# Optimization experiments

Measured on AMD Instinct MI355X. Metric: run time of the kernel, lower is better.

The kernel has to match this reference:

```python
import jax, jax.numpy as jnp
import numpy as np

NUM_FEATURE = 512
HIDDEN = 256
NUM_CLASSES = 10
L1 = 1e-4
ALPHA = 1e-3
BATCH = 65536


def setup_inputs() -> dict:
    key = jax.random.key(0)
    k = jax.random.split(key, 6)
    x = jax.random.normal(k[0], (BATCH, NUM_FEATURE), dtype=jnp.float32)
    y = jax.random.randint(k[1], (BATCH,), 0, NUM_CLASSES, dtype=jnp.int32)
    fc0 = jax.random.normal(k[2], (NUM_FEATURE, 512), dtype=jnp.float32) / NUM_FEATURE
    fc1 = jax.random.normal(k[3], (NUM_FEATURE, 512), dtype=jnp.float32) / NUM_FEATURE
    w = jax.random.normal(k[4], (NUM_FEATURE, HIDDEN), dtype=jnp.float32) / NUM_FEATURE
    w1 = jax.random.normal(k[5], (HIDDEN, NUM_CLASSES), dtype=jnp.float32) / HIDDEN
    return {"x": x, "y": y, "fc0": fc0, "fc1": fc1, "w": w, "w1": w1}


def reference(x, y, fc0, fc1, w, w1):
    # sigmoid-gated MLP block with residual
    x1 = x @ fc0                                   # [B, 512]
    x2 = jax.nn.relu(x @ fc1)                      # [B, 512]
    x4 = x + (1.0 + jax.nn.sigmoid(x1)) * x2       # [B, 512] residual

    # head (Dropout(p=0.0) is identity)
    logits = jax.nn.relu(x4 @ w) @ w1              # [B, 10]
    pred = jnp.argmax(logits, axis=1)

    # cross-entropy (mean over batch)
    logp = jax.nn.log_softmax(logits, axis=-1)
    ce = -jnp.mean(jnp.take_along_axis(logp, y[:, None].astype(jnp.int32), axis=1))

    # L1 penalty on all weight matrices
    l1_pen = L1 * (jnp.abs(w1).sum() + jnp.abs(w).sum()
                   + jnp.abs(fc0).sum() + jnp.abs(fc1).sum())

    # per-class variance: sum_i ||mean_{y_i} - x4_i||^2, vectorized via segment sums
    counts = jax.ops.segment_sum(jnp.ones((x4.shape[0],), jnp.float32), y,
                                 num_segments=NUM_CLASSES)
    sums = jax.ops.segment_sum(x4, y, num_segments=NUM_CLASSES)   # [10, 512]
    means = sums / jnp.maximum(counts, 1.0)[:, None]
    var_loss = jnp.sum(jnp.square(means[y] - x4))

    loss = ce + l1_pen + ALPHA * var_loss
    acc = jnp.mean((pred.astype(jnp.int32) == y.astype(jnp.int32)).astype(jnp.float32))
    return (loss, acc)
```

## Files before the change

### kernel.cpp

```cpp
#include <hip/hip_runtime.h>
#include <stdint.h>

#define BATCH 65536
#define FDIM 512
#define HDIM 256
#define NC 10
#define NREP 16

typedef short short8 __attribute__((ext_vector_type(8)));
typedef float f32x4 __attribute__((ext_vector_type(4)));

#define OFF_FC0T   ((size_t)0)
#define OFF_FC1T   (OFF_FC0T + (size_t)512*512*2)
#define OFF_WT     (OFF_FC1T + (size_t)512*512*2)
#define OFF_XT     (OFF_WT   + (size_t)256*512*2)
#define OFF_X4T    (OFF_XT   + (size_t)BATCH*512*2)
#define OFF_ACC    (OFF_X4T  + (size_t)BATCH*512*2)
#define SCAL_SUMSQ 0
#define SCAL_CE    16
#define SCAL_ACC   32
#define SCAL_L1    48
#define SCAL_N     128
#define CNT_OFF    SCAL_N
#define GSUM_OFF   (SCAL_N + NREP*16)
#define ACC_FLOATS (GSUM_OFF + NREP*5120)
#define OFF_W1T    (OFF_ACC + (size_t)ACC_FLOATS*4)

#define GLL(g,l) __builtin_amdgcn_global_load_lds((const __attribute__((address_space(1))) void*)(g), (__attribute__((address_space(3))) void*)(l), 16, 0, 0)

__device__ __forceinline__ unsigned short f2b(float f){
  unsigned u = __float_as_uint(f);
  u += 0x7FFFu + ((u >> 16) & 1u);
  return (unsigned short)(u >> 16);
}
__device__ __forceinline__ float b2f(unsigned short h){
  return __uint_as_float(((unsigned)h) << 16);
}
__device__ __forceinline__ unsigned pk2b(float f0, float f1){
  unsigned u0 = __float_as_uint(f0) + 0x8000u;
  unsigned u1 = __float_as_uint(f1) + 0x8000u;
  return __builtin_amdgcn_perm(u1, u0, 0x07060302u);
}

__global__ __launch_bounds__(256) void k_setup(
    const float* __restrict__ x,   const float* __restrict__ fc0,
    const float* __restrict__ fc1, const float* __restrict__ w,
    const float* __restrict__ w1,
    unsigned short* __restrict__ xT,   unsigned short* __restrict__ fc0T,
    unsigned short* __restrict__ fc1T, unsigned short* __restrict__ wT,
    unsigned short* __restrict__ w1T,  float* __restrict__ accb)
{
  int blk = blockIdx.x, t = threadIdx.x;
  if (blk < 1024){
    int I = blk*4 + (t >> 6);
    int l = t & 63;
    int row = I*16 + (l & 15), q = l >> 4;
    const float* src = x + (size_t)row*FDIM + q*8;
    #pragma unroll
    for (int C = 0; C < 16; ++C){
      float4 v0 = *(const float4*)(src + C*32);
      float4 v1 = *(const float4*)(src + C*32 + 4);
      unsigned o[4];
      o[0] = pk2b(v0.x, v0.y); o[1] = pk2b(v0.z, v0.w);
      o[2] = pk2b(v1.x, v1.y); o[3] = pk2b(v1.z, v1.w);
      *(short8*)&xT[(((size_t)I*16 + C) << 9) + l*8] = *(short8*)o;
    }
    return;
  }
  if (blk < 1360){
    int i = (blk - 1024)*256 + t;
    float l1v = 0.f;
    if (i < 32768){
      int n4 = i&15, m = (i>>4)&3, C = (i>>6)&15, J = i>>10;
      int n = J*16+n4, k8 = C*4+m;
      unsigned short o[8];
      #pragma unroll
      for (int j=0;j<8;++j){ float v = fc0[(size_t)(k8*8+j)*512 + n]; o[j]=f2b(v); l1v += fabsf(v); }
      *(short8*)&fc0T[(size_t)(J*16+C)*512 + (i&63)*8] = *(short8*)o;
    } else if (i < 65536){
      int j0 = i - 32768;
      int n4 = j0&15, m = (j0>>4)&3, C = (j0>>6)&15, J = j0>>10;
      int n = J*16+n4, k8 = C*4+m;
      unsigned short o[8];
      #pragma unroll
      for (int j=0;j<8;++j){ float v = fc1[(size_t)(k8*8+j)*512 + n]; o[j]=f2b(v); l1v += fabsf(v); }
      *(short8*)&fc1T[(size_t)(J*16+C)*512 + (j0&63)*8] = *(short8*)o;
    } else if (i < 81920){
      int j0 = i - 65536;
      int n4 = j0&15, m = (j0>>4)&3, C = (j0>>6)&15, J = j0>>10;
      int n = J*16+n4, k8 = C*4+m;
      unsigned short o[8];
      #pragma unroll
      for (int j=0;j<8;++j){ float v = w[(size_t)(k8*8+j)*256 + n]; o[j]=f2b(v); l1v += fabsf(v); }
      *(short8*)&wT[(size_t)(J*16+C)*512 + (j0&63)*8] = *(short8*)o;
    } else if (i < 86016){
      int j0 = i - 81920;
      int C = j0 >> 9, l = (j0 >> 3) & 63, e = j0 & 7;
      int n = l & 15, k = C*32 + (l>>4)*8 + e;
      float v = (n < NC) ? w1[k*NC + n] : 0.f;
      w1T[C*512 + l*8 + e] = f2b(v);
      if (n < NC) l1v = fabsf(v);
    }
    for (int off = 32; off; off >>= 1) l1v += __shfl_down(l1v, off);
    if ((t & 63) == 0 && l1v != 0.f)
      atomicAdd(&accb[SCAL_L1 + (blk & (NREP-1))], l1v);
    return;
  }
  {
    int base = (blk - 1360)*1024;
    #pragma unroll
    for (int j=0;j<4;++j){
      int idx = base + j*256 + t;
      if (idx < ACC_FLOATS) accb[idx] = 0.f;
    }
  }
}


#define BARRIER() __builtin_amdgcn_s_barrier()
#define LGKM0() do{ asm volatile("s_waitcnt lgkmcnt(0)" ::: "memory"); \
                    __builtin_amdgcn_sched_barrier(0); }while(0)

#define READA(A, AB, H) do{                                                   \
  _Pragma("unroll") for (int c_=0;c_<2;++c_)                                  \
  _Pragma("unroll") for (int m_=0;m_<4;++m_)                                  \
    A[c_][m_] = *(const short8*)((AB) + (((wr*8 + (H)*4 + m_)*2 + c_)<<10) + lane*16); \
}while(0)

#define READB(B, BB, MAT) do{                                                 \
  _Pragma("unroll") for (int c_=0;c_<2;++c_)                                  \
  _Pragma("unroll") for (int n_=0;n_<2;++n_)                                  \
    B[c_][n_] = *(const short8*)((BB) + (MAT)*16384 + (((wc*2+n_)*2 + c_)<<10) + lane*16); \
}while(0)

#define MM(ACC, MB, A, B) do{                                                 \
  __builtin_amdgcn_s_setprio(1);                                              \
  _Pragma("unroll") for (int c_=0;c_<2;++c_)                                  \
  _Pragma("unroll") for (int n_=0;n_<2;++n_)                                  \
  _Pragma("unroll") for (int m_=0;m_<4;++m_)                                  \
    ACC[(MB)+m_][n_] = __builtin_amdgcn_mfma_f32_16x16x32_bf16(A[c_][m_], B[c_][n_], ACC[(MB)+m_][n_], 0,0,0); \
  __builtin_amdgcn_s_setprio(0);                                              \
}while(0)

#define STAGEA(KT2, H) do{                                                    \
  char* d_ = ldsd + (((KT2)&1) ? 65536 : 0);                                  \
  _Pragma("unroll") for (int r_=0;r_<2;++r_){                                 \
    int idx_ = r_*8 + wv, q_ = idx_>>1, C_ = idx_&1;                          \
    int Il_ = (q_&3) + ((q_>>2)<<3) + (H)*4;                                  \
    GLL(xb + (((size_t)((rowblk*16 + Il_)*16 + (KT2)*2 + C_)) << 10) + lane*16, \
        d_ + ((Il_*2 + C_) << 10) + lane*16);                                 \
  } }while(0)

#define STAGEB(KT2, MAT) do{                                                  \
  char* d_ = ldsd + (((KT2)&1) ? 65536 : 0) + 32768 + (MAT)*16384;            \
  const char* s_ = (MAT) ? b1b : b0b;                                         \
  _Pragma("unroll") for (int r_=0;r_<2;++r_){                                 \
    int idx_ = r_*8 + wv, J_ = idx_>>1, C_ = idx_&1;                          \
    GLL(s_ + (((size_t)((colblk*8 + J_)*16 + (KT2)*2 + C_)) << 10) + lane*16, \
        d_ + ((J_*2 + C_) << 10) + lane*16);                                  \
  } }while(0)

__global__ __launch_bounds__(512, 2) void k_gemm12(
    const unsigned short* __restrict__ xT,
    const unsigned short* __restrict__ fc0T,
    const unsigned short* __restrict__ fc1T,
    unsigned short* __restrict__ x4T,
    float* __restrict__ scal)
{
  extern __shared__ __align__(16) char ldsd[];

  int blk = blockIdx.x;
  int wg = (blk & 7)*128 + (blk >> 3);
  int rowblk = wg >> 2;
  int colblk = wg & 3;

  int t = threadIdx.x;
  int wv = t >> 6, lane = t & 63, ln = lane & 15, quad = lane >> 4;
  int wr = wv >> 2, wc = wv & 3;

  const char* xb  = (const char*)xT;
  const char* b0b = (const char*)fc0T;
  const char* b1b = (const char*)fc1T;

  const f32x4 zv = {0.f,0.f,0.f,0.f};
  f32x4 acc1[8][2], acc2[8][2];
  #pragma unroll
  for (int m=0;m<8;++m){ acc1[m][0]=zv; acc1[m][1]=zv; acc2[m][0]=zv; acc2[m][1]=zv; }

  STAGEA(0,0); STAGEA(0,1); STAGEB(0,0); STAGEB(0,1);
  STAGEB(1,0); STAGEA(1,1);
  asm volatile("s_waitcnt vmcnt(4)" ::: "memory");
  __builtin_amdgcn_sched_barrier(0);
  BARRIER();

  short8 a0[2][4], a1[2][4], bb[2][2];

  for (int kt = 0; kt < 8; ++kt){
    char* Ab = ldsd + ((kt&1) ? 65536 : 0);
    char* Bb = Ab + 32768;

    READA(a0, Ab, 0);
    READB(bb, Bb, 0);
    if (kt < 7) STAGEA(kt+1, 0);
    BARRIER(); LGKM0();
    MM(acc1, 0, a0, bb);
    BARRIER();

    READA(a1, Ab, 1);
    if (kt < 7) STAGEB(kt+1, 1);
    BARRIER(); LGKM0();
    MM(acc1, 4, a1, bb);
    BARRIER();

    READB(bb, Bb, 1);
    if (kt < 6) STAGEB(kt+2, 0);
    BARRIER(); LGKM0();
    MM(acc2, 4, a1, bb);
    BARRIER();

    READA(a0, Ab, 0);
    if (kt < 6) STAGEA(kt+2, 1);
    BARRIER(); LGKM0();
    MM(acc2, 0, a0, bb);
    if (kt < 6)       { asm volatile("s_waitcnt vmcnt(4)" ::: "memory"); }
    else if (kt == 6) { asm volatile("s_waitcnt vmcnt(0)" ::: "memory"); }
    __builtin_amdgcn_sched_barrier(0);
    BARRIER();
  }

  {
    int Cres = colblk*4 + wc;
    #pragma unroll
    for (int i = 0; i < 8; ++i){
      GLL(xb + (((size_t)((rowblk*16 + wr*8 + i)*16 + Cres)) << 10) + lane*16,
          ldsd + ((wv*8 + i) << 10) + lane*16);
    }
    asm volatile("s_waitcnt vmcnt(0)" ::: "memory");
  }
  __syncthreads();

  unsigned short* resU = (unsigned short*)ldsd;
  unsigned short* x4U  = (unsigned short*)(ldsd + 65536);
  float sumsq = 0.f;
  #pragma unroll
  for (int m = 0; m < 8; ++m){
    #pragma unroll
    for (int n = 0; n < 2; ++n){
      #pragma unroll
      for (int r = 0; r < 4; ++r){
        int slot = (quad*4 + r) | ((n*2 + (ln>>3)) << 4);
        int idx = ((wv*8 + m) << 9) + slot*8 + (ln & 7);
        float xv  = b2f(resU[idx]);
        float x1v = acc1[m][n][r];
        float x2v = fmaxf(acc2[m][n][r], 0.f);
        float gate = 1.f + 1.f/(1.f + __expf(-x1v));
        float x4v = fmaf(gate, x2v, xv);
        unsigned short ub = f2b(x4v);
        float fq = b2f(ub);
        sumsq = fmaf(fq, fq, sumsq);
        x4U[idx] = ub;
      }
    }
  }
  for (int off = 32; off; off >>= 1) sumsq += __shfl_down(sumsq, off);
  __syncthreads();
  float* red = (float*)ldsd;
  if (lane == 0) red[wv] = sumsq;
  __syncthreads();
  if (t == 0){
    float s = 0.f;
    #pragma unroll
    for (int i=0;i<8;++i) s += red[i];
    atomicAdd(&scal[SCAL_SUMSQ + (blk & (NREP-1))], s);
  }
  #pragma unroll
  for (int r = 0; r < 2; ++r){
    int o = r*512 + t;
    int tile = o >> 6, off16 = o & 63;
    int wvp = tile >> 3, i = tile & 7;
    size_t Ig = (size_t)rowblk*16 + (wvp>>2)*8 + i;
    int Cg = colblk*4 + (wvp & 3);
    *(short8*)&x4T[((Ig*16 + Cg) << 9) + off16*8] =
      *(const short8*)&x4U[(tile << 9) + off16*8];
  }
}

__global__ __launch_bounds__(256) void k_csum(const unsigned short* __restrict__ x4T,
                                              const int* __restrict__ y,
                                              float* __restrict__ gsum){
  int w = blockIdx.x*4 + (threadIdx.x >> 6);
  int l = threadIdx.x & 63;
  int C = w & 15, Ig = w >> 4;
  int rl = l & 15, q = l >> 4;
  float a[NC][8];
  #pragma unroll
  for (int c=0;c<NC;++c)
    #pragma unroll
    for (int e=0;e<8;++e) a[c][e]=0.f;
  for (int ii = 0; ii < 64; ++ii){
    int I = Ig*64 + ii;
    int yv = y[I*16 + rl];
    short8 v = *(const short8*)&x4T[(((size_t)I*16 + C) << 9) + l*8];
    float f[8];
    #pragma unroll
    for (int e=0;e<8;++e) f[e] = b2f((unsigned short)v[e]);
    #pragma unroll
    for (int c=0;c<NC;++c){
      bool m = (yv == c);
      #pragma unroll
      for (int e=0;e<8;++e) a[c][e] += m ? f[e] : 0.f;
    }
  }
  #pragma unroll
  for (int off = 1; off < 16; off <<= 1)
    #pragma unroll
    for (int c=0;c<NC;++c)
      #pragma unroll
      for (int e=0;e<8;++e) a[c][e] += __shfl_xor(a[c][e], off);
  if (rl == 0){
    int rep = Ig & (NREP-1);
    int kb = C*32 + q*8;
    #pragma unroll
    for (int c=0;c<NC;++c)
      #pragma unroll
      for (int e=0;e<8;++e)
        atomicAdd(&gsum[(size_t)rep*5120 + c*512 + kb + e], a[c][e]);
  }
}

__global__ __launch_bounds__(256) void k_cnt(const int* __restrict__ y,
                                             float* __restrict__ gcnt){
  __shared__ float cntS[NC];
  int t = threadIdx.x;
  if (t < NC) cntS[t] = 0.f;
  __syncthreads();
  int base = blockIdx.x*2048;
  for (int i = t; i < 2048; i += 256) atomicAdd(&cntS[y[base+i]], 1.f);
  __syncthreads();
  if (t < NC) atomicAdd(&gcnt[(blockIdx.x & (NREP-1))*16 + t], cntS[t]);
}

__global__ __launch_bounds__(512) void k_gemm3_head(
    const unsigned short* __restrict__ x4T,
    const unsigned short* __restrict__ wT,
    const unsigned short* __restrict__ w1T,
    const int* __restrict__ y,
    float* __restrict__ scal)
{
  __shared__ __align__(16) char lds[49152];
  unsigned short* As     = (unsigned short*)lds;
  unsigned short* Bs     = (unsigned short*)(lds + 16384);
  unsigned short* transH = (unsigned short*)lds;
  __shared__ __align__(16) unsigned short w1s[4096];
  __shared__ float redc[8], reda[8];

  int blk = blockIdx.x;
  int t = threadIdx.x;
  int wv = t >> 6, lane = t & 63, ln = lane & 15, quad = lane >> 4;
  int wr = wv >> 2, wc = wv & 3;
  int rep = (blk ^ (blk >> 4)) & (NREP-1);

  *(short8*)&w1s[t*8] = *(const short8*)&w1T[t*8];

  const f32x4 zv = {0.f,0.f,0.f,0.f};
  f32x4 acc[4][4];
  #pragma unroll
  for (int rt=0;rt<4;++rt)
    #pragma unroll
    for (int ct=0;ct<4;++ct) acc[rt][ct] = zv;

  const char* ab = (const char*)x4T;
  const char* bb = (const char*)wT;

  for (int kt = 0; kt < 8; ++kt){
    {
      size_t Ig = (size_t)(blk*8 + wv);
      GLL(ab + ((Ig*16 + kt*2 + 0) << 10) + lane*16, (char*)As + ((wv*2+0) << 10));
      GLL(ab + ((Ig*16 + kt*2 + 1) << 10) + lane*16, (char*)As + ((wv*2+1) << 10));
    }
    #pragma unroll
    for (int i = 0; i < 2; ++i)
      #pragma unroll
      for (int c = 0; c < 2; ++c){
        size_t Jg = (size_t)(wv*2 + i);
        GLL(bb + ((Jg*16 + kt*2 + c) << 10) + lane*16,
            (char*)Bs + (((wv*2+i)*2 + c) << 10));
      }
    __syncthreads();
    #pragma unroll
    for (int c = 0; c < 2; ++c){
      short8 a[4];
      #pragma unroll
      for (int rt=0;rt<4;++rt)
        a[rt] = *(const short8*)&As[(((wr*4+rt)*2 + c) << 9) + lane*8];
      #pragma unroll
      for (int ct=0;ct<4;++ct){
        short8 b = *(const short8*)&Bs[(((wc*4+ct)*2 + c) << 9) + lane*8];
        #pragma unroll
        for (int rt=0;rt<4;++rt)
          acc[rt][ct] = __builtin_amdgcn_mfma_f32_16x16x32_bf16(a[rt], b, acc[rt][ct], 0,0,0);
      }
    }
    __syncthreads();
  }

  f32x4 alog = zv;
  #pragma unroll
  for (int hf = 0; hf < 2; ++hf){
    __syncthreads();
    if ((wc >> 1) == hf){
      #pragma unroll
      for (int rt=0;rt<4;++rt)
        #pragma unroll
        for (int ct=0;ct<4;++ct)
          #pragma unroll
          for (int r=0;r<4;++r){
            int row_l = wr*64 + rt*16 + quad*4 + r;
            int ch = (wc & 1)*64 + ct*16 + ln;
            int tile = ((row_l >> 4) << 2) | (ch >> 5);
            int slot = (row_l & 15) | (((ch >> 3) & 3) << 4);
            transH[(tile << 9) + slot*8 + (ch & 7)] = f2b(fmaxf(acc[rt][ct][r], 0.f));
          }
    }
    __syncthreads();
    #pragma unroll
    for (int Cl = 0; Cl < 4; ++Cl){
      short8 a = *(const short8*)&transH[((wv*4 + Cl) << 9) + lane*8];
      short8 b = *(const short8*)&w1s[(hf*4 + Cl)*512 + lane*8];
      alog = __builtin_amdgcn_mfma_f32_16x16x32_bf16(a, b, alog, 0,0,0);
    }
  }

  float ce_l = 0.f, acc_l = 0.f;
  #pragma unroll
  for (int r = 0; r < 4; ++r){
    int grow = blk*128 + wv*16 + quad*4 + r;
    int yv = y[grow];
    float lg = (ln < NC) ? alog[r] : -1e30f;
    float m = lg; int mi = ln;
    #pragma unroll
    for (int mk = 1; mk < 16; mk <<= 1){
      float om = __shfl_xor(m, mk); int oi = __shfl_xor(mi, mk);
      if (om > m || (om == m && oi < mi)){ m = om; mi = oi; }
    }
    float e  = (ln < NC) ? __expf(lg - m) : 0.f;
    float sy = (ln == yv) ? lg : 0.f;
    #pragma unroll
    for (int mk = 1; mk < 16; mk <<= 1){ e += __shfl_xor(e, mk); sy += __shfl_xor(sy, mk); }
    float lse = m + __logf(e);
    if (ln == 0){ ce_l += (lse - sy); acc_l += (mi == yv) ? 1.f : 0.f; }
  }
  ce_l  += __shfl_down(ce_l, 16);  acc_l += __shfl_down(acc_l, 16);
  ce_l  += __shfl_down(ce_l, 32);  acc_l += __shfl_down(acc_l, 32);
  if (lane == 0){ redc[wv] = ce_l; reda[wv] = acc_l; }
  __syncthreads();
  if (t == 0){
    float c = 0.f, a = 0.f;
    #pragma unroll
    for (int i=0;i<8;++i){ c += redc[i]; a += reda[i]; }
    atomicAdd(&scal[SCAL_CE  + rep], c);
    atomicAdd(&scal[SCAL_ACC + rep], a);
  }
}

__global__ __launch_bounds__(1024) void k_final(const float* __restrict__ accb,
                                                float* __restrict__ out){
  const float* gsum = accb + GSUM_OFF;
  const float* gcnt = accb + CNT_OFF;
  int t = threadIdx.x;
  float contrib = 0.f;
  for (int idx = t; idx < 5120; idx += 1024){
    float S = 0.f;
    #pragma unroll
    for (int r = 0; r < NREP; ++r) S += gsum[(size_t)r*5120 + idx];
    int c = idx >> 9;
    float cnt = 0.f;
    #pragma unroll
    for (int r = 0; r < NREP; ++r) cnt += gcnt[r*16 + c];
    contrib += S*S / fmaxf(cnt, 1.f);
  }
  for (int off = 32; off; off >>= 1) contrib += __shfl_down(contrib, off);
  __shared__ float red[16];
  if ((t & 63) == 0) red[t >> 6] = contrib;
  __syncthreads();
  if (t == 0){
    float var2 = 0.f;
    #pragma unroll
    for (int i=0;i<16;++i) var2 += red[i];
    float sumsq=0.f, ce=0.f, acc=0.f, l1=0.f;
    for (int r=0;r<NREP;++r){
      sumsq += accb[SCAL_SUMSQ+r];
      ce    += accb[SCAL_CE+r];
      acc   += accb[SCAL_ACC+r];
      l1    += accb[SCAL_L1+r];
    }
    float var_loss = sumsq - var2;
    out[0] = ce/(float)BATCH + 1e-4f*l1 + 1e-3f*var_loss;
    out[1] = acc/(float)BATCH;
  }
}

extern "C" void kernel_launch(void* const* d_in, const int* in_sizes, int n_in,
                              void* d_out, int out_size, void* d_ws, size_t ws_size,
                              hipStream_t stream){
  (void)in_sizes; (void)n_in; (void)out_size; (void)ws_size;
  const float* x   = (const float*)d_in[0];
  const int*   y   = (const int*)d_in[1];
  const float* fc0 = (const float*)d_in[2];
  const float* fc1 = (const float*)d_in[3];
  const float* w   = (const float*)d_in[4];
  const float* w1  = (const float*)d_in[5];
  char* ws = (char*)d_ws;
  unsigned short* fc0T = (unsigned short*)(ws + OFF_FC0T);
  unsigned short* fc1T = (unsigned short*)(ws + OFF_FC1T);
  unsigned short* wT   = (unsigned short*)(ws + OFF_WT);
  unsigned short* xT   = (unsigned short*)(ws + OFF_XT);
  unsigned short* x4T  = (unsigned short*)(ws + OFF_X4T);
  unsigned short* w1T  = (unsigned short*)(ws + OFF_W1T);
  float* accb = (float*)(ws + OFF_ACC);
  float* scal = accb;
  float* gcnt = accb + CNT_OFF;
  float* gsum = accb + GSUM_OFF;

  static bool once = [](){
    hipFuncSetAttribute((const void*)k_gemm12,
                        hipFuncAttributeMaxDynamicSharedMemorySize, 131072);
    return true;
  }();
  (void)once;

  k_setup<<<1441, 256, 0, stream>>>(x, fc0, fc1, w, w1, xT, fc0T, fc1T, wT, w1T, accb);
  k_gemm12<<<1024, 512, 131072, stream>>>(xT, fc0T, fc1T, x4T, scal);
  k_cnt<<<32, 256, 0, stream>>>(y, gcnt);
  k_csum<<<256, 256, 0, stream>>>(x4T, y, gsum);
  k_gemm3_head<<<512, 512, 0, stream>>>(x4T, wT, w1T, y, scal);
  k_final<<<1, 1024, 0, stream>>>(accb, (float*)d_out);
}
```

Baseline: 404.5 us.

## Reuse pipelined gemm12 k-loop for head GEMM and fold class counting into setup

```diff
diff --git a/kernel.cpp b/kernel.cpp
--- a/kernel.cpp
+++ b/kernel.cpp
@@ -45,7 +45,7 @@
 __global__ __launch_bounds__(256) void k_setup(
     const float* __restrict__ x,   const float* __restrict__ fc0,
     const float* __restrict__ fc1, const float* __restrict__ w,
-    const float* __restrict__ w1,
+    const float* __restrict__ w1,  const int* __restrict__ y,
     unsigned short* __restrict__ xT,   unsigned short* __restrict__ fc0T,
     unsigned short* __restrict__ fc1T, unsigned short* __restrict__ wT,
     unsigned short* __restrict__ w1T,  float* __restrict__ accb)
@@ -106,13 +106,25 @@
       atomicAdd(&accb[SCAL_L1 + (blk & (NREP-1))], l1v);
     return;
   }
-  {
+  if (blk < 1441){
     int base = (blk - 1360)*1024;
     #pragma unroll
     for (int j=0;j<4;++j){
       int idx = base + j*256 + t;
-      if (idx < ACC_FLOATS) accb[idx] = 0.f;
-    }
+      if (idx < ACC_FLOATS && (idx < CNT_OFF || idx >= CNT_OFF + NREP*16))
+        accb[idx] = 0.f;
+    }
+    return;
+  }
+  {
+    __shared__ float cntS[16];
+    int b = blk - 1441;
+    if (t < 16) cntS[t] = 0.f;
+    __syncthreads();
+    int base = b*4096;
+    for (int i = t; i < 4096; i += 256) atomicAdd(&cntS[y[base+i]], 1.f);
+    __syncthreads();
+    if (t < 16) accb[CNT_OFF + b*16 + t] = cntS[t];
   }
 }
 
@@ -133,12 +145,16 @@
     B[c_][n_] = *(const short8*)((BB) + (MAT)*16384 + (((wc*2+n_)*2 + c_)<<10) + lane*16); \
 }while(0)
 
-#define MM(ACC, MB, A, B) do{                                                 \
+#define MMALL(MB) do{                                                         \
   __builtin_amdgcn_s_setprio(1);                                              \
   _Pragma("unroll") for (int c_=0;c_<2;++c_)                                  \
   _Pragma("unroll") for (int n_=0;n_<2;++n_)                                  \
   _Pragma("unroll") for (int m_=0;m_<4;++m_)                                  \
-    ACC[(MB)+m_][n_] = __builtin_amdgcn_mfma_f32_16x16x32_bf16(A[c_][m_], B[c_][n_], ACC[(MB)+m_][n_], 0,0,0); \
+    acc1[(MB)+m_][n_] = __builtin_amdgcn_mfma_f32_16x16x32_bf16(a[c_][m_], b0[c_][n_], acc1[(MB)+m_][n_], 0,0,0); \
+  _Pragma("unroll") for (int c_=0;c_<2;++c_)                                  \
+  _Pragma("unroll") for (int n_=0;n_<2;++n_)                                  \
+  _Pragma("unroll") for (int m_=0;m_<4;++m_)                                  \
+    acc2[(MB)+m_][n_] = __builtin_amdgcn_mfma_f32_16x16x32_bf16(a[c_][m_], b1[c_][n_], acc2[(MB)+m_][n_], 0,0,0); \
   __builtin_amdgcn_s_setprio(0);                                              \
 }while(0)
 
@@ -160,6 +176,36 @@
         d_ + ((J_*2 + C_) << 10) + lane*16);                                  \
   } }while(0)
 
+#define KLOOP_PROLOGUE() do{                                                  \
+  STAGEA(0,0); STAGEA(0,1); STAGEB(0,0); STAGEB(0,1);                         \
+  STAGEA(1,0); STAGEB(1,0);                                                   \
+  asm volatile("s_waitcnt vmcnt(4)" ::: "memory");                            \
+  __builtin_amdgcn_sched_barrier(0);                                          \
+  BARRIER();                                                                  \
+}while(0)
+
+#define KLOOP_BODY(kt) do{                                                    \
+  char* Ab = ldsd + (((kt)&1) ? 65536 : 0);                                   \
+  char* Bb = Ab + 32768;                                                      \
+                                                                      \
+  READA(a, Ab, 0);                                                            \
+  READB(b0, Bb, 0);                                                           \
+  READB(b1, Bb, 1);                                                           \
+  if ((kt) < 7){ STAGEA((kt)+1, 1); STAGEB((kt)+1, 1); }                      \
+  BARRIER(); LGKM0();                                                         \
+  MMALL(0);                                                                   \
+  BARRIER();                                                                  \
+                                                                      \
+  READA(a, Ab, 1);                                                            \
+  if ((kt) < 6){ STAGEA((kt)+2, 0); STAGEB((kt)+2, 0); }                      \
+  BARRIER(); LGKM0();                                                         \
+  MMALL(4);                                                                   \
+  if ((kt) < 6)       { asm volatile("s_waitcnt vmcnt(4)" ::: "memory"); }    \
+  else if ((kt) == 6) { asm volatile("s_waitcnt vmcnt(0)" ::: "memory"); }    \
+  __builtin_amdgcn_sched_barrier(0);                                          \
+  BARRIER();                                                                  \
+}while(0)
+
 __global__ __launch_bounds__(512, 2) void k_gemm12(
     const unsigned short* __restrict__ xT,
     const unsigned short* __restrict__ fc0T,
@@ -187,46 +233,10 @@
   #pragma unroll
   for (int m=0;m<8;++m){ acc1[m][0]=zv; acc1[m][1]=zv; acc2[m][0]=zv; acc2[m][1]=zv; }
 
-  STAGEA(0,0); STAGEA(0,1); STAGEB(0,0); STAGEB(0,1);
-  STAGEB(1,0); STAGEA(1,1);
-  asm volatile("s_waitcnt vmcnt(4)" ::: "memory");
-  __builtin_amdgcn_sched_barrier(0);
-  BARRIER();
-
-  short8 a0[2][4], a1[2][4], bb[2][2];
-
-  for (int kt = 0; kt < 8; ++kt){
-    char* Ab = ldsd + ((kt&1) ? 65536 : 0);
-    char* Bb = Ab + 32768;
-
-    READA(a0, Ab, 0);
-    READB(bb, Bb, 0);
-    if (kt < 7) STAGEA(kt+1, 0);
-    BARRIER(); LGKM0();
-    MM(acc1, 0, a0, bb);
-    BARRIER();
-
-    READA(a1, Ab, 1);
-    if (kt < 7) STAGEB(kt+1, 1);
-    BARRIER(); LGKM0();
-    MM(acc1, 4, a1, bb);
-    BARRIER();
-
-    READB(bb, Bb, 1);
-    if (kt < 6) STAGEB(kt+2, 0);
-    BARRIER(); LGKM0();
-    MM(acc2, 4, a1, bb);
-    BARRIER();
-
-    READA(a0, Ab, 0);
-    if (kt < 6) STAGEA(kt+2, 1);
-    BARRIER(); LGKM0();
-    MM(acc2, 0, a0, bb);
-    if (kt < 6)       { asm volatile("s_waitcnt vmcnt(4)" ::: "memory"); }
-    else if (kt == 6) { asm volatile("s_waitcnt vmcnt(0)" ::: "memory"); }
-    __builtin_amdgcn_sched_barrier(0);
-    BARRIER();
-  }
+  short8 a[2][4], b0[2][2], b1[2][2];
+
+  KLOOP_PROLOGUE();
+  for (int kt = 0; kt < 8; ++kt) KLOOP_BODY(kt);
 
   {
     int Cres = colblk*4 + wc;
@@ -328,138 +338,104 @@
   }
 }
 
-__global__ __launch_bounds__(256) void k_cnt(const int* __restrict__ y,
-                                             float* __restrict__ gcnt){
-  __shared__ float cntS[NC];
-  int t = threadIdx.x;
-  if (t < NC) cntS[t] = 0.f;
-  __syncthreads();
-  int base = blockIdx.x*2048;
-  for (int i = t; i < 2048; i += 256) atomicAdd(&cntS[y[base+i]], 1.f);
-  __syncthreads();
-  if (t < NC) atomicAdd(&gcnt[(blockIdx.x & (NREP-1))*16 + t], cntS[t]);
-}
-
-__global__ __launch_bounds__(512) void k_gemm3_head(
+__global__ __launch_bounds__(512, 2) void k_gemm3_head(
     const unsigned short* __restrict__ x4T,
     const unsigned short* __restrict__ wT,
     const unsigned short* __restrict__ w1T,
     const int* __restrict__ y,
     float* __restrict__ scal)
 {
-  __shared__ __align__(16) char lds[49152];
-  unsigned short* As     = (unsigned short*)lds;
-  unsigned short* Bs     = (unsigned short*)(lds + 16384);
-  unsigned short* transH = (unsigned short*)lds;
-  __shared__ __align__(16) unsigned short w1s[4096];
+  extern __shared__ __align__(16) char ldsd[];
   __shared__ float redc[8], reda[8];
 
   int blk = blockIdx.x;
+  int rowblk = blk;
+  const int colblk = 0;
+
   int t = threadIdx.x;
   int wv = t >> 6, lane = t & 63, ln = lane & 15, quad = lane >> 4;
   int wr = wv >> 2, wc = wv & 3;
   int rep = (blk ^ (blk >> 4)) & (NREP-1);
 
-  *(short8*)&w1s[t*8] = *(const short8*)&w1T[t*8];
+  const char* xb  = (const char*)x4T;
+  const char* b0b = (const char*)wT;
+  const char* b1b = (const char*)wT + (size_t)128*1024;
 
   const f32x4 zv = {0.f,0.f,0.f,0.f};
-  f32x4 acc[4][4];
-  #pragma unroll
-  for (int rt=0;rt<4;++rt)
-    #pragma unroll
-    for (int ct=0;ct<4;++ct) acc[rt][ct] = zv;
-
-  const char* ab = (const char*)x4T;
-  const char* bb = (const char*)wT;
-
-  for (int kt = 0; kt < 8; ++kt){
-    {
-      size_t Ig = (size_t)(blk*8 + wv);
-      GLL(ab + ((Ig*16 + kt*2 + 0) << 10) + lane*16, (char*)As + ((wv*2+0) << 10));
-      GLL(ab + ((Ig*16 + kt*2 + 1) << 10) + lane*16, (char*)As + ((wv*2+1) << 10));
-    }
-    #pragma unroll
-    for (int i = 0; i < 2; ++i)
-      #pragma unroll
-      for (int c = 0; c < 2; ++c){
-        size_t Jg = (size_t)(wv*2 + i);
-        GLL(bb + ((Jg*16 + kt*2 + c) << 10) + lane*16,
-            (char*)Bs + (((wv*2+i)*2 + c) << 10));
+  f32x4 acc1[8][2], acc2[8][2];
+  #pragma unroll
+  for (int m=0;m<8;++m){ acc1[m][0]=zv; acc1[m][1]=zv; acc2[m][0]=zv; acc2[m][1]=zv; }
+
+  short8 a[2][4], b0[2][2], b1[2][2];
+
+  KLOOP_PROLOGUE();
+  for (int kt = 0; kt < 8; ++kt) KLOOP_BODY(kt);
+
+  short8 bw1[8];
+  #pragma unroll
+  for (int Ck = 0; Ck < 8; ++Ck)
+    bw1[Ck] = *(const short8*)&w1T[Ck*512 + lane*8];
+
+  unsigned short* transH = (unsigned short*)ldsd;
+  #pragma unroll
+  for (int m = 0; m < 8; ++m){
+    #pragma unroll
+    for (int n = 0; n < 2; ++n){
+      #pragma unroll
+      for (int r = 0; r < 4; ++r){
+        int slot = (quad*4 + r) | ((n*2 + (ln>>3)) << 4);
+        int e = ln & 7;
+        int IhA = wr*8 + m;
+        transH[((IhA*8 + wc)     << 9) + slot*8 + e] = f2b(fmaxf(acc1[m][n][r], 0.f));
+        transH[((IhA*8 + 4 + wc) << 9) + slot*8 + e] = f2b(fmaxf(acc2[m][n][r], 0.f));
       }
-    __syncthreads();
-    #pragma unroll
-    for (int c = 0; c < 2; ++c){
-      short8 a[4];
-      #pragma unroll
-      for (int rt=0;rt<4;++rt)
-        a[rt] = *(const short8*)&As[(((wr*4+rt)*2 + c) << 9) + lane*8];
-      #pragma unroll
-      for (int ct=0;ct<4;++ct){
-        short8 b = *(const short8*)&Bs[(((wc*4+ct)*2 + c) << 9) + lane*8];
-        #pragma unroll
-        for (int rt=0;rt<4;++rt)
-          acc[rt][ct] = __builtin_amdgcn_mfma_f32_16x16x32_bf16(a[rt], b, acc[rt][ct], 0,0,0);
+    }
+  }
+  __syncthreads();
+
+  f32x4 alog[2] = {zv, zv};
+  #pragma unroll
+  for (int ih = 0; ih < 2; ++ih){
+    int Ih = wv*2 + ih;
+    #pragma unroll
+    for (int Ck = 0; Ck < 8; ++Ck){
+      short8 af = *(const short8*)&transH[((Ih*8 + Ck) << 9) + lane*8];
+      alog[ih] = __builtin_amdgcn_mfma_f32_16x16x32_bf16(af, bw1[Ck], alog[ih], 0,0,0);
+    }
+  }
+
+  float ce_l = 0.f, acc_l = 0.f;
+  #pragma unroll
+  for (int ih = 0; ih < 2; ++ih){
+    #pragma unroll
+    for (int r = 0; r < 4; ++r){
+      int grow = blk*256 + (wv*2 + ih)*16 + quad*4 + r;
+      int yv = y[grow];
+      float lg = (ln < NC) ? alog[ih][r] : -1e30f;
+      float m = lg; int mi = ln;
+      #pragma unroll
+      for (int mk = 1; mk < 16; mk <<= 1){
+        float om = __shfl_xor(m, mk); int oi = __shfl_xor(mi, mk);
+        if (om > m || (om == m && oi < mi)){ m = om; mi = oi; }
       }
-    }
-    __syncthreads();
-  }
-
-  f32x4 alog = zv;
-  #pragma unroll
-  for (int hf = 0; hf < 2; ++hf){
-    __syncthreads();
-    if ((wc >> 1) == hf){
-      #pragma unroll
-      for (int rt=0;rt<4;++rt)
-        #pragma unroll
-        for (int ct=0;ct<4;++ct)
-          #pragma unroll
-          for (int r=0;r<4;++r){
-            int row_l = wr*64 + rt*16 + quad*4 + r;
-            int ch = (wc & 1)*64 + ct*16 + ln;
-            int tile = ((row_l >> 4) << 2) | (ch >> 5);
-            int slot = (row_l & 15) | (((ch >> 3) & 3) << 4);
-            transH[(tile << 9) + slot*8 + (ch & 7)] = f2b(fmaxf(acc[rt][ct][r], 0.f));
-          }
-    }
-    __syncthreads();
-    #pragma unroll
-    for (int Cl = 0; Cl < 4; ++Cl){
-      short8 a = *(const short8*)&transH[((wv*4 + Cl) << 9) + lane*8];
-      short8 b = *(const short8*)&w1s[(hf*4 + Cl)*512 + lane*8];
-      alog = __builtin_amdgcn_mfma_f32_16x16x32_bf16(a, b, alog, 0,0,0);
-    }
-  }
-
-  float ce_l = 0.f, acc_l = 0.f;
-  #pragma unroll
-  for (int r = 0; r < 4; ++r){
-    int grow = blk*128 + wv*16 + quad*4 + r;
-    int yv = y[grow];
-    float lg = (ln < NC) ? alog[r] : -1e30f;
-    float m = lg; int mi = ln;
-    #pragma unroll
-    for (int mk = 1; mk < 16; mk <<= 1){
-      float om = __shfl_xor(m, mk); int oi = __shfl_xor(mi, mk);
-      if (om > m || (om == m && oi < mi)){ m = om; mi = oi; }
-    }
-    float e  = (ln < NC) ? __expf(lg - m) : 0.f;
-    float sy = (ln == yv) ? lg : 0.f;
-    #pragma unroll
-    for (int mk = 1; mk < 16; mk <<= 1){ e += __shfl_xor(e, mk); sy += __shfl_xor(sy, mk); }
-    float lse = m + __logf(e);
-    if (ln == 0){ ce_l += (lse - sy); acc_l += (mi == yv) ? 1.f : 0.f; }
+      float e  = (ln < NC) ? __expf(lg - m) : 0.f;
+      float sy = (ln == yv) ? lg : 0.f;
+      #pragma unroll
+      for (int mk = 1; mk < 16; mk <<= 1){ e += __shfl_xor(e, mk); sy += __shfl_xor(sy, mk); }
+      float lse = m + __logf(e);
+      if (ln == 0){ ce_l += (lse - sy); acc_l += (mi == yv) ? 1.f : 0.f; }
+    }
   }
   ce_l  += __shfl_down(ce_l, 16);  acc_l += __shfl_down(acc_l, 16);
   ce_l  += __shfl_down(ce_l, 32);  acc_l += __shfl_down(acc_l, 32);
   if (lane == 0){ redc[wv] = ce_l; reda[wv] = acc_l; }
   __syncthreads();
   if (t == 0){
-    float c = 0.f, a = 0.f;
-    #pragma unroll
-    for (int i=0;i<8;++i){ c += redc[i]; a += reda[i]; }
+    float c = 0.f, aa = 0.f;
+    #pragma unroll
+    for (int i=0;i<8;++i){ c += redc[i]; aa += reda[i]; }
     atomicAdd(&scal[SCAL_CE  + rep], c);
-    atomicAdd(&scal[SCAL_ACC + rep], a);
+    atomicAdd(&scal[SCAL_ACC + rep], aa);
   }
 }
 
@@ -519,20 +495,20 @@
   unsigned short* w1T  = (unsigned short*)(ws + OFF_W1T);
   float* accb = (float*)(ws + OFF_ACC);
   float* scal = accb;
-  float* gcnt = accb + CNT_OFF;
   float* gsum = accb + GSUM_OFF;
 
   static bool once = [](){
     hipFuncSetAttribute((const void*)k_gemm12,
+                        hipFuncAttributeMaxDynamicSharedMemorySize, 131072);
+    hipFuncSetAttribute((const void*)k_gemm3_head,
                         hipFuncAttributeMaxDynamicSharedMemorySize, 131072);
     return true;
   }();
   (void)once;
 
-  k_setup<<<1441, 256, 0, stream>>>(x, fc0, fc1, w, w1, xT, fc0T, fc1T, wT, w1T, accb);
+  k_setup<<<1457, 256, 0, stream>>>(x, fc0, fc1, w, w1, y, xT, fc0T, fc1T, wT, w1T, accb);
   k_gemm12<<<1024, 512, 131072, stream>>>(xT, fc0T, fc1T, x4T, scal);
-  k_cnt<<<32, 256, 0, stream>>>(y, gcnt);
   k_csum<<<256, 256, 0, stream>>>(x4T, y, gsum);
-  k_gemm3_head<<<512, 512, 0, stream>>>(x4T, wT, w1T, y, scal);
+  k_gemm3_head<<<256, 512, 131072, stream>>>(x4T, wT, w1T, y, scal);
   k_final<<<1, 1024, 0, stream>>>(accb, (float*)d_out);
 }
```

New measurement: 399.3 us. About the same (-1.3%).
